# Optimization experiments

Measured on AMD Instinct MI355X. Metric: run time of the kernel, lower is better.

Reference implementation:

```python
import jax, jax.numpy as jnp
import numpy as np

B, N, D, H = 8, 1024, 512, 8  # batch, num_nodes, dim, num_heads
HD = D // H                    # head_dim = 64
N_VALID = 896                  # last 128 nodes per graph are padding


def setup_inputs() -> dict:
    key = jax.random.key(0)
    ks = jax.random.split(key, 6)
    x = jax.random.normal(ks[0], (B, N, D), dtype=jnp.float32)
    # boolean validity mask: some padding nodes so mask-fill / nan_to_num paths are hit
    mask = np.ones((B, N), dtype=bool)
    mask[:, N_VALID:] = False
    node_valid_mask = jnp.asarray(mask)
    attn_bias = jax.random.normal(ks[1], (B, H, N, N), dtype=jnp.float32) * 0.1
    # torch nn.Linear convention: y = x @ W.T + b
    qkv_w = jax.random.normal(ks[2], (3 * D, D), dtype=jnp.float32) * (D ** -0.5)
    qkv_b = jax.random.normal(ks[3], (3 * D,), dtype=jnp.float32) * 0.02
    out_w = jax.random.normal(ks[4], (D, D), dtype=jnp.float32) * (D ** -0.5)
    out_b = jax.random.normal(ks[5], (D,), dtype=jnp.float32) * 0.02
    return {"x": x, "node_valid_mask": node_valid_mask, "attn_bias": attn_bias,
            "qkv_w": qkv_w, "qkv_b": qkv_b, "out_w": out_w, "out_b": out_b}


def reference(x, node_valid_mask, attn_bias, qkv_w, qkv_b, out_w, out_b):
    b, n, d = x.shape
    scale = HD ** -0.5
    # qkv projection -> [3, B, H, N, HD]
    qkv = (x @ qkv_w.T + qkv_b).reshape(b, n, 3, H, HD).transpose(2, 0, 3, 1, 4)
    q, k, v = qkv[0], qkv[1], qkv[2]
    scores = jnp.einsum('bhqd,bhkd->bhqk', q, k) * scale + attn_bias  # [B,H,N,N]
    # pair mask: both query and key node must be valid
    pair_mask = node_valid_mask[:, :, None] & node_valid_mask[:, None, :]  # [B,N,N]
    scores = jnp.where(pair_mask[:, None, :, :], scores, -jnp.inf)
    attn = jax.nn.softmax(scores, axis=-1)
    # fully-masked query rows produce NaN -> zero, matching torch.nan_to_num
    attn = jnp.nan_to_num(attn, nan=0.0, posinf=0.0, neginf=0.0)
    out = jnp.einsum('bhqk,bhkd->bhqd', attn, v)        # [B,H,N,HD]
    out = out.transpose(0, 2, 1, 3).reshape(b, n, d)     # [B,N,D]
    return out @ out_w.T + out_b
```

## Files before the change

kernel.cpp:

```cpp
#include <hip/hip_runtime.h>
#include <math.h>

constexpr int Bc  = 8;
constexpr int Nn  = 1024;
constexpr int Dd  = 512;
constexpr int Hh  = 8;
constexpr int HD  = 64;
constexpr float SCALE = 0.125f;

typedef unsigned short ushort_t;
typedef unsigned int uint32;
typedef __attribute__((ext_vector_type(8))) short short8;
typedef __attribute__((ext_vector_type(4))) float f32x4;

__device__ __forceinline__ uint32 bf16rn(float x) {
  uint32 u = __float_as_uint(x);
  return (u + 0x7FFFu + ((u >> 16) & 1u)) >> 16;
}
__device__ __forceinline__ float bf16up(uint32 h) { return __uint_as_float(h << 16); }

__device__ __forceinline__ void split8(const float* xs, uint4& hi, uint4& lo) {
  uint32 h[8], l[8];
#pragma unroll
  for (int j = 0; j < 8; ++j) {
    h[j] = bf16rn(xs[j]);
    l[j] = bf16rn(xs[j] - bf16up(h[j]));
  }
  hi.x = h[0] | (h[1] << 16); hi.y = h[2] | (h[3] << 16);
  hi.z = h[4] | (h[5] << 16); hi.w = h[6] | (h[7] << 16);
  lo.x = l[0] | (l[1] << 16); lo.y = l[2] | (l[3] << 16);
  lo.z = l[4] | (l[5] << 16); lo.w = l[6] | (l[7] << 16);
}

__device__ __forceinline__ bool lane_valid(const unsigned char* m8, bool bytelay, int idx) {
  if (bytelay) return m8[idx] != 0;
  return ((const int*)m8)[idx] != 0;
}

__global__ __launch_bounds__(256) void convert_split(
    const float* __restrict__ src, ushort_t* __restrict__ dst)
{
  const int t    = blockIdx.x * 256 + threadIdx.x;
  const int lane = t & 63;
  const int blk  = t >> 6;
  const int rt   = blk >> 4, ks = blk & 15;
  const int row  = rt * 16 + (lane & 15);
  const int k    = ks * 32 + (lane >> 4) * 8;

  const float* s = src + (size_t)row * 512 + k;
  float4 a = *(const float4*)s, b = *(const float4*)(s + 4);
  float xs[8] = {a.x, a.y, a.z, a.w, b.x, b.y, b.z, b.w};
  uint4 hi, lo; split8(xs, hi, lo);

  ushort_t* d = dst + (size_t)blk * 1024 + lane * 8;
  *(uint4*)d = hi;
  *(uint4*)(d + 512) = lo;
}

__global__ __launch_bounds__(256) void convert_frag_qk(
    const float* __restrict__ src, ushort_t* __restrict__ dst)
{
  const int t    = blockIdx.x * 256 + threadIdx.x;
  const int lane = t & 63;
  const int fid  = t >> 6;
  const int tile = fid >> 1, ks = fid & 1;
  const int row  = tile * 16 + (lane & 15);
  const int d    = ks * 32 + (lane >> 4) * 8;

  const float* s = src + (size_t)row * HD + d;
  float4 a = *(const float4*)s, b = *(const float4*)(s + 4);
  float xs[8] = {a.x, a.y, a.z, a.w, b.x, b.y, b.z, b.w};
  uint4 hi, lo; split8(xs, hi, lo);

  ushort_t* dp = dst + (size_t)fid * 1024 + lane * 8;
  *(uint4*)dp = hi;
  *(uint4*)(dp + 512) = lo;
}

__global__ __launch_bounds__(256) void convert_frag_v(
    const float* __restrict__ src, ushort_t* __restrict__ dst)
{
  const int t    = blockIdx.x * 256 + threadIdx.x;
  const int lane = t & 63;
  const int fid  = t >> 6;
  const int dt   = fid & 3;
  const int ks   = (fid >> 2) & 1;
  const int kt   = (fid >> 3) & 15;
  const int bh   = fid >> 7;
  const int d    = dt * 16 + (lane & 15);
  const int key0 = kt * 64 + ks * 32 + (lane >> 4) * 8;

  const float* s = src + ((size_t)bh * Nn + key0) * HD + d;
  float xs[8];
#pragma unroll
  for (int j = 0; j < 8; ++j) xs[j] = s[(size_t)j * HD];
  uint4 hi, lo; split8(xs, hi, lo);

  ushort_t* dp = dst + (size_t)fid * 1024 + lane * 8;
  *(uint4*)dp = hi;
  *(uint4*)(dp + 512) = lo;
}

template<bool SCATTER>
__global__ __launch_bounds__(256) void gemm_x3(
    const ushort_t* __restrict__ Ac, const float* __restrict__ W,
    const float* __restrict__ bias, float* __restrict__ C, int Ncols,
    float* __restrict__ qb, float* __restrict__ kb, float* __restrict__ vb)
{
  __shared__ ushort_t Ablk[8 * 1024];
  __shared__ ushort_t Bblk[8 * 1024];

  const int t    = threadIdx.x;
  const int lane = t & 63, w = t >> 6;
  const int wr   = w >> 1, wc = w & 1;
  const int j0   = blockIdx.x * 128, i0 = blockIdx.y * 128;
  const int srow = t >> 2, skc = t & 3;

  f32x4 acc[4][4];
#pragma unroll
  for (int a = 0; a < 4; ++a)
#pragma unroll
    for (int b = 0; b < 4; ++b) acc[a][b] = (f32x4){0.f, 0.f, 0.f, 0.f};

  for (int kt = 0; kt < 16; ++kt) {
    __syncthreads();
#pragma unroll
    for (int i = 0; i < 4; ++i) {
      const int c = w * 4 + i, rt = c >> 1, hl = c & 1;
      const size_t goff =
          ((size_t)((i0 >> 4) + rt) * 16 + kt) * 1024 + hl * 512 + lane * 8;
      *(uint4*)&Ablk[rt * 1024 + hl * 512 + lane * 8] = *(const uint4*)&Ac[goff];
    }
#pragma unroll
    for (int p = 0; p < 2; ++p) {
      const int row = p * 64 + srow;
      const float* s = W + (size_t)(j0 + row) * 512 + kt * 32 + skc * 8;
      float4 w0 = *(const float4*)s, w1 = *(const float4*)(s + 4);
      float xs[8] = {w0.x, w0.y, w0.z, w0.w, w1.x, w1.y, w1.z, w1.w};
      uint4 hi, lo; split8(xs, hi, lo);
      ushort_t* d = &Bblk[(row >> 4) * 1024 + ((row & 15) + 16 * skc) * 8];
      *(uint4*)d = hi;
      *(uint4*)(d + 512) = lo;
    }
    __syncthreads();

    const ushort_t* Ab = &Ablk[(wr * 4) * 1024 + lane * 8];
    const ushort_t* Bb = &Bblk[(wc * 4) * 1024 + lane * 8];
    short8 Ah[4], Al[4];
#pragma unroll
    for (int ti = 0; ti < 4; ++ti) {
      Ah[ti] = *(const short8*)(Ab + ti * 1024);
      Al[ti] = *(const short8*)(Ab + ti * 1024 + 512);
    }
#pragma unroll
    for (int ct = 0; ct < 4; ++ct) {
      short8 Bh = *(const short8*)(Bb + ct * 1024);
      short8 Bl = *(const short8*)(Bb + ct * 1024 + 512);
#pragma unroll
      for (int ti = 0; ti < 4; ++ti) {
        acc[ti][ct] = __builtin_amdgcn_mfma_f32_16x16x32_bf16(Ah[ti], Bh, acc[ti][ct], 0, 0, 0);
        acc[ti][ct] = __builtin_amdgcn_mfma_f32_16x16x32_bf16(Al[ti], Bh, acc[ti][ct], 0, 0, 0);
        acc[ti][ct] = __builtin_amdgcn_mfma_f32_16x16x32_bf16(Ah[ti], Bl, acc[ti][ct], 0, 0, 0);
      }
    }
  }

  const int rbase = i0 + wr * 64 + (lane >> 4) * 4;
  const int cbase = j0 + wc * 64 + (lane & 15);
#pragma unroll
  for (int ct = 0; ct < 4; ++ct) {
    const int col = cbase + ct * 16;
    const float bv = bias[col];
    float* dst = nullptr;
    if (SCATTER) {
      const int s = col >> 9, h = (col >> 6) & 7;
      dst  = (s == 0) ? qb : (s == 1) ? kb : vb;
      dst += (size_t)h * Nn * HD + (col & 63);
    }
#pragma unroll
    for (int ti = 0; ti < 4; ++ti) {
      const int r0 = rbase + ti * 16;
#pragma unroll
      for (int r = 0; r < 4; ++r) {
        const float v = acc[ti][ct][r] + bv;
        const int row = r0 + r;
        if (SCATTER) {
          const int b2 = row >> 10, n = row & 1023;
          dst[((size_t)b2 * Hh * Nn + n) * HD] = v;
        } else {
          C[(size_t)row * Ncols + col] = v;
        }
      }
    }
  }
}

__global__ __launch_bounds__(256) void attn_mfma(
    const ushort_t* __restrict__ qf, const ushort_t* __restrict__ kf,
    const ushort_t* __restrict__ vf, const float* __restrict__ bias,
    const unsigned char* __restrict__ m8, float* __restrict__ outp)
{
  __shared__ ushort_t Pbuf[4][2048];

  const int t    = threadIdx.x;
  const int lane = t & 63, w = t >> 6;
  const int bx   = blockIdx.x;
  const int qt   = bx & 15;
  const int bh   = bx >> 4;
  const int b    = bh >> 3, h = bh & 7;
  const int tt   = qt * 4 + w;
  const int q0   = tt * 16;
  const bool bytelay = (m8[1] != 0);

  short8 Qh[2], Ql[2];
#pragma unroll
  for (int ks = 0; ks < 2; ++ks) {
    const ushort_t* qp = qf + ((size_t)(bh * 64 + tt) * 2 + ks) * 1024 + lane * 8;
    Qh[ks] = *(const short8*)qp;
    Ql[ks] = *(const short8*)(qp + 512);
  }

  f32x4 Oacc[4];
#pragma unroll
  for (int dt = 0; dt < 4; ++dt) Oacc[dt] = (f32x4){0.f, 0.f, 0.f, 0.f};
  float m_run[4], l_run[4];
#pragma unroll
  for (int r = 0; r < 4; ++r) { m_run[r] = -__builtin_inff(); l_run[r] = 0.f; }

  ushort_t* pb = &Pbuf[w][0];

  for (int kt = 0; kt < 16; ++kt) {
    const bool kvme = lane_valid(m8, bytelay, b * Nn + kt * 64 + lane);
    const unsigned long long kmask = __ballot(kvme);
    if (kmask == 0ull) continue;

    const float* bp = bias + ((size_t)bh * Nn + q0 + (lane >> 4) * 4) * Nn
                           + kt * 64 + (lane & 15);
    float bias_v[4][4];
#pragma unroll
    for (int r = 0; r < 4; ++r)
#pragma unroll
      for (int nt = 0; nt < 4; ++nt)
        bias_v[nt][r] = bp[(size_t)r * Nn + nt * 16];

    f32x4 Sacc[4];
#pragma unroll
    for (int nt = 0; nt < 4; ++nt) Sacc[nt] = (f32x4){0.f, 0.f, 0.f, 0.f};
#pragma unroll
    for (int ks = 0; ks < 2; ++ks)
#pragma unroll
      for (int nt = 0; nt < 4; ++nt) {
        const ushort_t* kp =
            kf + ((size_t)(bh * 64 + kt * 4 + nt) * 2 + ks) * 1024 + lane * 8;
        short8 Kh = *(const short8*)kp;
        short8 Kl = *(const short8*)(kp + 512);
        Sacc[nt] = __builtin_amdgcn_mfma_f32_16x16x32_bf16(Qh[ks], Kh, Sacc[nt], 0, 0, 0);
        Sacc[nt] = __builtin_amdgcn_mfma_f32_16x16x32_bf16(Ql[ks], Kh, Sacc[nt], 0, 0, 0);
        Sacc[nt] = __builtin_amdgcn_mfma_f32_16x16x32_bf16(Qh[ks], Kl, Sacc[nt], 0, 0, 0);
      }

    float Sv[4][4];
    float mt[4] = {-__builtin_inff(), -__builtin_inff(), -__builtin_inff(), -__builtin_inff()};
#pragma unroll
    for (int nt = 0; nt < 4; ++nt) {
      const bool kv = (kmask >> (nt * 16 + (lane & 15))) & 1ull;
#pragma unroll
      for (int r = 0; r < 4; ++r) {
        float s = kv ? Sacc[nt][r] * SCALE + bias_v[nt][r] : -__builtin_inff();
        Sv[nt][r] = s;
        mt[r] = fmaxf(mt[r], s);
      }
    }
#pragma unroll
    for (int off = 1; off < 16; off <<= 1)
#pragma unroll
      for (int r = 0; r < 4; ++r) mt[r] = fmaxf(mt[r], __shfl_xor(mt[r], off));

    float alpha[4], lt[4];
#pragma unroll
    for (int r = 0; r < 4; ++r) {
      const float mn = fmaxf(m_run[r], mt[r]);
      alpha[r] = __expf(m_run[r] - mn);
      m_run[r] = mn;
      lt[r] = 0.f;
    }
#pragma unroll
    for (int nt = 0; nt < 4; ++nt) {
      const int ksp    = nt >> 1;
      const int key_in = (nt & 1) * 16 + (lane & 15);
      const int lane_p = 16 * (key_in >> 3);
      const int j      = key_in & 7;
#pragma unroll
      for (int r = 0; r < 4; ++r) {
        const float p = __expf(Sv[nt][r] - m_run[r]);
        lt[r] += p;
        const uint32 ph = bf16rn(p);
        const uint32 pl = bf16rn(p - bf16up(ph));
        const int lp = ((lane >> 4) * 4 + r) + lane_p;
        pb[(ksp * 2 + 0) * 512 + lp * 8 + j] = (ushort_t)ph;
        pb[(ksp * 2 + 1) * 512 + lp * 8 + j] = (ushort_t)pl;
      }
    }
#pragma unroll
    for (int off = 1; off < 16; off <<= 1)
#pragma unroll
      for (int r = 0; r < 4; ++r) lt[r] += __shfl_xor(lt[r], off);
#pragma unroll
    for (int r = 0; r < 4; ++r) l_run[r] = l_run[r] * alpha[r] + lt[r];
#pragma unroll
    for (int dt = 0; dt < 4; ++dt)
#pragma unroll
      for (int r = 0; r < 4; ++r) Oacc[dt][r] *= alpha[r];

    short8 Ph[2], Pl[2];
#pragma unroll
    for (int ks = 0; ks < 2; ++ks) {
      Ph[ks] = *(const short8*)&pb[(ks * 2 + 0) * 512 + lane * 8];
      Pl[ks] = *(const short8*)&pb[(ks * 2 + 1) * 512 + lane * 8];
    }

#pragma unroll
    for (int dt = 0; dt < 4; ++dt)
#pragma unroll
      for (int ks = 0; ks < 2; ++ks) {
        const ushort_t* vp =
            vf + ((size_t)(((bh * 16 + kt) * 2 + ks) * 4 + dt)) * 1024 + lane * 8;
        short8 Vh = *(const short8*)vp;
        short8 Vl = *(const short8*)(vp + 512);
        Oacc[dt] = __builtin_amdgcn_mfma_f32_16x16x32_bf16(Ph[ks], Vh, Oacc[dt], 0, 0, 0);
        Oacc[dt] = __builtin_amdgcn_mfma_f32_16x16x32_bf16(Pl[ks], Vh, Oacc[dt], 0, 0, 0);
        Oacc[dt] = __builtin_amdgcn_mfma_f32_16x16x32_bf16(Ph[ks], Vl, Oacc[dt], 0, 0, 0);
      }
  }

#pragma unroll
  for (int r = 0; r < 4; ++r) {
    const int q = q0 + (lane >> 4) * 4 + r;
    const bool vq = lane_valid(m8, bytelay, b * Nn + q);
    const float rinv = (vq && l_run[r] > 0.f) ? (1.f / l_run[r]) : 0.f;
    float* op = outp + ((size_t)(b * Nn + q)) * Dd + h * HD + (lane & 15);
#pragma unroll
    for (int dt = 0; dt < 4; ++dt) op[dt * 16] = Oacc[dt][r] * rinv;
  }
}

extern "C" void kernel_launch(void* const* d_in, const int* in_sizes, int n_in,
                              void* d_out, int out_size, void* d_ws, size_t ws_size,
                              hipStream_t stream) {
  const float* x        = (const float*)d_in[0];
  const unsigned char* mask8 = (const unsigned char*)d_in[1];
  const float* attnbias = (const float*)d_in[2];
  const float* qkv_w    = (const float*)d_in[3];
  const float* qkv_b    = (const float*)d_in[4];
  const float* out_w    = (const float*)d_in[5];
  const float* out_b    = (const float*)d_in[6];
  float* out = (float*)d_out;

  float* ws = (float*)d_ws;
  const size_t SEG = (size_t)Bc * Hh * Nn * HD;
  float* A = ws;
  float* B = ws + SEG;
  float* C = ws + 2 * SEG;
  float* D = ws + 3 * SEG;

  ushort_t* x_conv    = (ushort_t*)A;
  float*    qbuf      = B;
  float*    kbuf      = C;
  float*    vbuf      = D;
  ushort_t* qfrag     = (ushort_t*)A;
  ushort_t* kfrag     = (ushort_t*)B;
  ushort_t* vfrag     = (ushort_t*)C;
  float*    aout      = D;
  ushort_t* aout_conv = (ushort_t*)A;

  convert_split<<<2048, 256, 0, stream>>>(x, x_conv);

  gemm_x3<true><<<dim3(12, 64), 256, 0, stream>>>(
      x_conv, qkv_w, qkv_b, nullptr, 1536, qbuf, kbuf, vbuf);

  convert_frag_qk<<<2048, 256, 0, stream>>>(qbuf, qfrag);
  convert_frag_qk<<<2048, 256, 0, stream>>>(kbuf, kfrag);
  convert_frag_v <<<2048, 256, 0, stream>>>(vbuf, vfrag);

  attn_mfma<<<1024, 256, 0, stream>>>(
      qfrag, kfrag, vfrag, attnbias, mask8, aout);

  convert_split<<<2048, 256, 0, stream>>>(aout, aout_conv);
  gemm_x3<false><<<dim3(4, 64), 256, 0, stream>>>(
      aout_conv, out_w, out_b, out, 512, nullptr, nullptr, nullptr);
}
```

Before: 566.9 us.

## Pre-split weights into bf16 fragments, prefetch attention bias, narrow output GEMM tile

Weights are now converted once per call into hi/lo bf16 fragment layout by convert_split, so the GEMM inner loop only copies pre-split fragments instead of re-splitting fp32 weights in every block. The attention kernel prefetches the next key tile's bias with coalesced float4 loads into registers and stages it through shared memory, replacing strided scalar bias loads. The output GEMM uses a 64-wide column tile, which gives 512 blocks instead of 256. The cost is extra conversion launches and scratch use of d_out and workspace for the weight fragments.

Result: slower. 741.3 us (+30.8%).

```diff
diff --git a/kernel.cpp b/kernel.cpp
--- a/kernel.cpp
+++ b/kernel.cpp
@@ -101,51 +101,48 @@
   *(uint4*)(dp + 512) = lo;
 }
 
-template<bool SCATTER>
-__global__ __launch_bounds__(256) void gemm_x3(
-    const ushort_t* __restrict__ Ac, const float* __restrict__ W,
+template<int BN, bool SCATTER>
+__global__ __launch_bounds__(256) void gemm_f(
+    const ushort_t* __restrict__ Ac, const ushort_t* __restrict__ Bfrag,
     const float* __restrict__ bias, float* __restrict__ C, int Ncols,
     float* __restrict__ qb, float* __restrict__ kb, float* __restrict__ vb)
 {
-  __shared__ ushort_t Ablk[8 * 1024];
-  __shared__ ushort_t Bblk[8 * 1024];
-
-  const int t    = threadIdx.x;
-  const int lane = t & 63, w = t >> 6;
-  const int wr   = w >> 1, wc = w & 1;
-  const int j0   = blockIdx.x * 128, i0 = blockIdx.y * 128;
-  const int srow = t >> 2, skc = t & 3;
-
-  f32x4 acc[4][4];
+  constexpr int NT   = BN / 32;
+  constexpr int BCH  = (BN / 16) * 2;
+  __shared__ ushort_t Ablk[16 * 512];
+  __shared__ ushort_t Bblk[BCH * 512];
+
+  const int t = threadIdx.x, lane = t & 63, w = t >> 6;
+  const int wr = w >> 1, wc = w & 1;
+  const int j0 = blockIdx.x * BN, i0 = blockIdx.y * 128;
+
+  f32x4 acc[4][NT];
 #pragma unroll
   for (int a = 0; a < 4; ++a)
 #pragma unroll
-    for (int b = 0; b < 4; ++b) acc[a][b] = (f32x4){0.f, 0.f, 0.f, 0.f};
+    for (int b = 0; b < NT; ++b) acc[a][b] = (f32x4){0.f, 0.f, 0.f, 0.f};
 
   for (int kt = 0; kt < 16; ++kt) {
     __syncthreads();
 #pragma unroll
-    for (int i = 0; i < 4; ++i) {
-      const int c = w * 4 + i, rt = c >> 1, hl = c & 1;
-      const size_t goff =
-          ((size_t)((i0 >> 4) + rt) * 16 + kt) * 1024 + hl * 512 + lane * 8;
-      *(uint4*)&Ablk[rt * 1024 + hl * 512 + lane * 8] = *(const uint4*)&Ac[goff];
-    }
-#pragma unroll
-    for (int p = 0; p < 2; ++p) {
-      const int row = p * 64 + srow;
-      const float* s = W + (size_t)(j0 + row) * 512 + kt * 32 + skc * 8;
-      float4 w0 = *(const float4*)s, w1 = *(const float4*)(s + 4);
-      float xs[8] = {w0.x, w0.y, w0.z, w0.w, w1.x, w1.y, w1.z, w1.w};
-      uint4 hi, lo; split8(xs, hi, lo);
-      ushort_t* d = &Bblk[(row >> 4) * 1024 + ((row & 15) + 16 * skc) * 8];
-      *(uint4*)d = hi;
-      *(uint4*)(d + 512) = lo;
+    for (int ci = 0; ci < (16 + BCH) / 4; ++ci) {
+      const int c = ci * 4 + w;
+      const ushort_t* src;
+      ushort_t* dst;
+      if (c < 16) {
+        const int rt = c >> 1, hl = c & 1;
+        src = Ac + (((size_t)((i0 >> 4) + rt) * 16 + kt)) * 1024 + hl * 512 + lane * 8;
+        dst = Ablk + c * 512 + lane * 8;
+      } else {
+        const int cb = c - 16, bt = cb >> 1, hl = cb & 1;
+        src = Bfrag + (((size_t)((j0 >> 4) + bt) * 16 + kt)) * 1024 + hl * 512 + lane * 8;
+        dst = Bblk + cb * 512 + lane * 8;
+      }
+      *(uint4*)dst = *(const uint4*)src;
     }
     __syncthreads();
 
-    const ushort_t* Ab = &Ablk[(wr * 4) * 1024 + lane * 8];
-    const ushort_t* Bb = &Bblk[(wc * 4) * 1024 + lane * 8];
+    const ushort_t* Ab = Ablk + (size_t)(wr * 4) * 1024 + lane * 8;
     short8 Ah[4], Al[4];
 #pragma unroll
     for (int ti = 0; ti < 4; ++ti) {
@@ -153,9 +150,10 @@
       Al[ti] = *(const short8*)(Ab + ti * 1024 + 512);
     }
 #pragma unroll
-    for (int ct = 0; ct < 4; ++ct) {
-      short8 Bh = *(const short8*)(Bb + ct * 1024);
-      short8 Bl = *(const short8*)(Bb + ct * 1024 + 512);
+    for (int ct = 0; ct < NT; ++ct) {
+      const ushort_t* Bb = Bblk + (size_t)(wc * NT + ct) * 1024 + lane * 8;
+      short8 Bh = *(const short8*)Bb;
+      short8 Bl = *(const short8*)(Bb + 512);
 #pragma unroll
       for (int ti = 0; ti < 4; ++ti) {
         acc[ti][ct] = __builtin_amdgcn_mfma_f32_16x16x32_bf16(Ah[ti], Bh, acc[ti][ct], 0, 0, 0);
@@ -166,10 +164,10 @@
   }
 
   const int rbase = i0 + wr * 64 + (lane >> 4) * 4;
-  const int cbase = j0 + wc * 64 + (lane & 15);
-#pragma unroll
-  for (int ct = 0; ct < 4; ++ct) {
-    const int col = cbase + ct * 16;
+  const int cb0   = j0 + wc * (NT * 16) + (lane & 15);
+#pragma unroll
+  for (int ct = 0; ct < NT; ++ct) {
+    const int col = cb0 + ct * 16;
     const float bv = bias[col];
     float* dst = nullptr;
     if (SCATTER) {
@@ -200,16 +198,14 @@
     const ushort_t* __restrict__ vf, const float* __restrict__ bias,
     const unsigned char* __restrict__ m8, float* __restrict__ outp)
 {
-  __shared__ ushort_t Pbuf[4][2048];
-
-  const int t    = threadIdx.x;
-  const int lane = t & 63, w = t >> 6;
-  const int bx   = blockIdx.x;
-  const int qt   = bx & 15;
-  const int bh   = bx >> 4;
-  const int b    = bh >> 3, h = bh & 7;
-  const int tt   = qt * 4 + w;
-  const int q0   = tt * 16;
+  __shared__ float sbuf[4][2][1088];
+
+  const int t = threadIdx.x, lane = t & 63, w = t >> 6;
+  const int bx = blockIdx.x;
+  const int qt = bx & 15, bh = bx >> 4;
+  const int b = bh >> 3, h = bh & 7;
+  const int tt = qt * 4 + w;
+  const int q0 = tt * 16;
   const bool bytelay = (m8[1] != 0);
 
   short8 Qh[2], Ql[2];
@@ -227,110 +223,134 @@
 #pragma unroll
   for (int r = 0; r < 4; ++r) { m_run[r] = -__builtin_inff(); l_run[r] = 0.f; }
 
-  ushort_t* pb = &Pbuf[w][0];
+  float*    bb = &sbuf[w][0][0];
+  ushort_t* pb = (ushort_t*)&sbuf[w][1][0];
+
+  const float* bp0 = bias + ((size_t)bh * Nn + q0 + (lane >> 4) * 4) * Nn + (lane & 15) * 4;
+
+  unsigned long long km_cur = __ballot(lane_valid(m8, bytelay, b * Nn + lane));
+  float4 breg[4] = {};
+  if (km_cur) {
+#pragma unroll
+    for (int i = 0; i < 4; ++i) breg[i] = *(const float4*)(bp0 + (size_t)i * Nn);
+  }
 
   for (int kt = 0; kt < 16; ++kt) {
-    const bool kvme = lane_valid(m8, bytelay, b * Nn + kt * 64 + lane);
-    const unsigned long long kmask = __ballot(kvme);
-    if (kmask == 0ull) continue;
-
-    const float* bp = bias + ((size_t)bh * Nn + q0 + (lane >> 4) * 4) * Nn
-                           + kt * 64 + (lane & 15);
-    float bias_v[4][4];
-#pragma unroll
-    for (int r = 0; r < 4; ++r)
+    unsigned long long km_next = 0ull;
+    if (kt < 15)
+      km_next = __ballot(lane_valid(m8, bytelay, b * Nn + (kt + 1) * 64 + lane));
+    float4 bnext[4] = {};
+    if (km_next) {
+      const float* bp = bp0 + (size_t)(kt + 1) * 64;
+#pragma unroll
+      for (int i = 0; i < 4; ++i) bnext[i] = *(const float4*)(bp + (size_t)i * Nn);
+    }
+
+    if (km_cur) {
+#pragma unroll
+      for (int i = 0; i < 4; ++i)
+        *(float4*)&bb[((lane >> 4) * 4 + i) * 68 + (lane & 15) * 4] = breg[i];
+
+      f32x4 Sacc[4];
+#pragma unroll
+      for (int nt = 0; nt < 4; ++nt) Sacc[nt] = (f32x4){0.f, 0.f, 0.f, 0.f};
+#pragma unroll
+      for (int ks = 0; ks < 2; ++ks)
+#pragma unroll
+        for (int nt = 0; nt < 4; ++nt) {
+          const ushort_t* kp =
+              kf + ((size_t)(bh * 64 + kt * 4 + nt) * 2 + ks) * 1024 + lane * 8;
+          short8 Kh = *(const short8*)kp;
+          short8 Kl = *(const short8*)(kp + 512);
+          Sacc[nt] = __builtin_amdgcn_mfma_f32_16x16x32_bf16(Qh[ks], Kh, Sacc[nt], 0, 0, 0);
+          Sacc[nt] = __builtin_amdgcn_mfma_f32_16x16x32_bf16(Ql[ks], Kh, Sacc[nt], 0, 0, 0);
+          Sacc[nt] = __builtin_amdgcn_mfma_f32_16x16x32_bf16(Qh[ks], Kl, Sacc[nt], 0, 0, 0);
+        }
+
+      float bias_v[4][4];
 #pragma unroll
       for (int nt = 0; nt < 4; ++nt)
-        bias_v[nt][r] = bp[(size_t)r * Nn + nt * 16];
-
-    f32x4 Sacc[4];
-#pragma unroll
-    for (int nt = 0; nt < 4; ++nt) Sacc[nt] = (f32x4){0.f, 0.f, 0.f, 0.f};
-#pragma unroll
-    for (int ks = 0; ks < 2; ++ks)
+#pragma unroll
+        for (int r = 0; r < 4; ++r)
+          bias_v[nt][r] = bb[((lane >> 4) * 4 + r) * 68 + nt * 16 + (lane & 15)];
+
+      float Sv[4][4];
+      float mt[4] = {-__builtin_inff(), -__builtin_inff(), -__builtin_inff(), -__builtin_inff()};
 #pragma unroll
       for (int nt = 0; nt < 4; ++nt) {
-        const ushort_t* kp =
-            kf + ((size_t)(bh * 64 + kt * 4 + nt) * 2 + ks) * 1024 + lane * 8;
-        short8 Kh = *(const short8*)kp;
-        short8 Kl = *(const short8*)(kp + 512);
-        Sacc[nt] = __builtin_amdgcn_mfma_f32_16x16x32_bf16(Qh[ks], Kh, Sacc[nt], 0, 0, 0);
-        Sacc[nt] = __builtin_amdgcn_mfma_f32_16x16x32_bf16(Ql[ks], Kh, Sacc[nt], 0, 0, 0);
-        Sacc[nt] = __builtin_amdgcn_mfma_f32_16x16x32_bf16(Qh[ks], Kl, Sacc[nt], 0, 0, 0);
-      }
-
-    float Sv[4][4];
-    float mt[4] = {-__builtin_inff(), -__builtin_inff(), -__builtin_inff(), -__builtin_inff()};
-#pragma unroll
-    for (int nt = 0; nt < 4; ++nt) {
-      const bool kv = (kmask >> (nt * 16 + (lane & 15))) & 1ull;
+        const bool kv = (km_cur >> (nt * 16 + (lane & 15))) & 1ull;
+#pragma unroll
+        for (int r = 0; r < 4; ++r) {
+          float s = kv ? Sacc[nt][r] * SCALE + bias_v[nt][r] : -__builtin_inff();
+          Sv[nt][r] = s;
+          mt[r] = fmaxf(mt[r], s);
+        }
+      }
+#pragma unroll
+      for (int off = 1; off < 16; off <<= 1)
+#pragma unroll
+        for (int r = 0; r < 4; ++r) mt[r] = fmaxf(mt[r], __shfl_xor(mt[r], off));
+
+      float alpha[4], lt[4];
 #pragma unroll
       for (int r = 0; r < 4; ++r) {
-        float s = kv ? Sacc[nt][r] * SCALE + bias_v[nt][r] : -__builtin_inff();
-        Sv[nt][r] = s;
-        mt[r] = fmaxf(mt[r], s);
-      }
-    }
-#pragma unroll
-    for (int off = 1; off < 16; off <<= 1)
-#pragma unroll
-      for (int r = 0; r < 4; ++r) mt[r] = fmaxf(mt[r], __shfl_xor(mt[r], off));
-
-    float alpha[4], lt[4];
-#pragma unroll
-    for (int r = 0; r < 4; ++r) {
-      const float mn = fmaxf(m_run[r], mt[r]);
-      alpha[r] = __expf(m_run[r] - mn);
-      m_run[r] = mn;
-      lt[r] = 0.f;
-    }
-#pragma unroll
-    for (int nt = 0; nt < 4; ++nt) {
-      const int ksp    = nt >> 1;
-      const int key_in = (nt & 1) * 16 + (lane & 15);
-      const int lane_p = 16 * (key_in >> 3);
-      const int j      = key_in & 7;
-#pragma unroll
-      for (int r = 0; r < 4; ++r) {
-        const float p = __expf(Sv[nt][r] - m_run[r]);
-        lt[r] += p;
-        const uint32 ph = bf16rn(p);
-        const uint32 pl = bf16rn(p - bf16up(ph));
-        const int lp = ((lane >> 4) * 4 + r) + lane_p;
-        pb[(ksp * 2 + 0) * 512 + lp * 8 + j] = (ushort_t)ph;
-        pb[(ksp * 2 + 1) * 512 + lp * 8 + j] = (ushort_t)pl;
-      }
-    }
-#pragma unroll
-    for (int off = 1; off < 16; off <<= 1)
-#pragma unroll
-      for (int r = 0; r < 4; ++r) lt[r] += __shfl_xor(lt[r], off);
-#pragma unroll
-    for (int r = 0; r < 4; ++r) l_run[r] = l_run[r] * alpha[r] + lt[r];
-#pragma unroll
-    for (int dt = 0; dt < 4; ++dt)
-#pragma unroll
-      for (int r = 0; r < 4; ++r) Oacc[dt][r] *= alpha[r];
-
-    short8 Ph[2], Pl[2];
-#pragma unroll
-    for (int ks = 0; ks < 2; ++ks) {
-      Ph[ks] = *(const short8*)&pb[(ks * 2 + 0) * 512 + lane * 8];
-      Pl[ks] = *(const short8*)&pb[(ks * 2 + 1) * 512 + lane * 8];
-    }
-
-#pragma unroll
-    for (int dt = 0; dt < 4; ++dt)
+        const float mn = fmaxf(m_run[r], mt[r]);
+        alpha[r] = __expf(m_run[r] - mn);
+        m_run[r] = mn;
+        lt[r] = 0.f;
+      }
+#pragma unroll
+      for (int nt = 0; nt < 4; ++nt) {
+        const int ksp    = nt >> 1;
+        const int key_in = (nt & 1) * 16 + (lane & 15);
+        const int lane_p = 16 * (key_in >> 3);
+        const int j      = key_in & 7;
+#pragma unroll
+        for (int r = 0; r < 4; ++r) {
+          const float p = __expf(Sv[nt][r] - m_run[r]);
+          lt[r] += p;
+          const uint32 ph = bf16rn(p);
+          const uint32 pl = bf16rn(p - bf16up(ph));
+          const int lp = ((lane >> 4) * 4 + r) + lane_p;
+          pb[(ksp * 2 + 0) * 512 + lp * 8 + j] = (ushort_t)ph;
+          pb[(ksp * 2 + 1) * 512 + lp * 8 + j] = (ushort_t)pl;
+        }
+      }
+#pragma unroll
+      for (int off = 1; off < 16; off <<= 1)
+#pragma unroll
+        for (int r = 0; r < 4; ++r) lt[r] += __shfl_xor(lt[r], off);
+#pragma unroll
+      for (int r = 0; r < 4; ++r) l_run[r] = l_run[r] * alpha[r] + lt[r];
+#pragma unroll
+      for (int dt = 0; dt < 4; ++dt)
+#pragma unroll
+        for (int r = 0; r < 4; ++r) Oacc[dt][r] *= alpha[r];
+
+      short8 Ph[2], Pl[2];
 #pragma unroll
       for (int ks = 0; ks < 2; ++ks) {
-        const ushort_t* vp =
-            vf + ((size_t)(((bh * 16 + kt) * 2 + ks) * 4 + dt)) * 1024 + lane * 8;
-        short8 Vh = *(const short8*)vp;
-        short8 Vl = *(const short8*)(vp + 512);
-        Oacc[dt] = __builtin_amdgcn_mfma_f32_16x16x32_bf16(Ph[ks], Vh, Oacc[dt], 0, 0, 0);
-        Oacc[dt] = __builtin_amdgcn_mfma_f32_16x16x32_bf16(Pl[ks], Vh, Oacc[dt], 0, 0, 0);
-        Oacc[dt] = __builtin_amdgcn_mfma_f32_16x16x32_bf16(Ph[ks], Vl, Oacc[dt], 0, 0, 0);
-      }
+        Ph[ks] = *(const short8*)&pb[(ks * 2 + 0) * 512 + lane * 8];
+        Pl[ks] = *(const short8*)&pb[(ks * 2 + 1) * 512 + lane * 8];
+      }
+
+#pragma unroll
+      for (int dt = 0; dt < 4; ++dt)
+#pragma unroll
+        for (int ks = 0; ks < 2; ++ks) {
+          const ushort_t* vp =
+              vf + ((size_t)(((bh * 16 + kt) * 2 + ks) * 4 + dt)) * 1024 + lane * 8;
+          short8 Vh = *(const short8*)vp;
+          short8 Vl = *(const short8*)(vp + 512);
+          Oacc[dt] = __builtin_amdgcn_mfma_f32_16x16x32_bf16(Ph[ks], Vh, Oacc[dt], 0, 0, 0);
+          Oacc[dt] = __builtin_amdgcn_mfma_f32_16x16x32_bf16(Pl[ks], Vh, Oacc[dt], 0, 0, 0);
+          Oacc[dt] = __builtin_amdgcn_mfma_f32_16x16x32_bf16(Ph[ks], Vl, Oacc[dt], 0, 0, 0);
+        }
+    }
+
+    km_cur = km_next;
+#pragma unroll
+    for (int i = 0; i < 4; ++i) breg[i] = bnext[i];
   }
 
 #pragma unroll
@@ -372,11 +392,14 @@
   ushort_t* vfrag     = (ushort_t*)C;
   float*    aout      = D;
   ushort_t* aout_conv = (ushort_t*)A;
+  ushort_t* qkv_wf    = (ushort_t*)d_out;
+  ushort_t* out_wf    = (ushort_t*)B;
 
   convert_split<<<2048, 256, 0, stream>>>(x, x_conv);
-
-  gemm_x3<true><<<dim3(12, 64), 256, 0, stream>>>(
-      x_conv, qkv_w, qkv_b, nullptr, 1536, qbuf, kbuf, vbuf);
+  convert_split<<<384, 256, 0, stream>>>(qkv_w, qkv_wf);
+
+  gemm_f<128, true><<<dim3(12, 64), 256, 0, stream>>>(
+      x_conv, qkv_wf, qkv_b, nullptr, 1536, qbuf, kbuf, vbuf);
 
   convert_frag_qk<<<2048, 256, 0, stream>>>(qbuf, qfrag);
   convert_frag_qk<<<2048, 256, 0, stream>>>(kbuf, kfrag);
@@ -385,7 +408,8 @@
   attn_mfma<<<1024, 256, 0, stream>>>(
       qfrag, kfrag, vfrag, attnbias, mask8, aout);
 
+  convert_split<<<128, 256, 0, stream>>>(out_w, out_wf);
   convert_split<<<2048, 256, 0, stream>>>(aout, aout_conv);
-  gemm_x3<false><<<dim3(4, 64), 256, 0, stream>>>(
-      aout_conv, out_w, out_b, out, 512, nullptr, nullptr, nullptr);
-}
+  gemm_f<64, false><<<dim3(8, 64), 256, 0, stream>>>(
+      aout_conv, out_wf, out_b, out, 512, nullptr, nullptr, nullptr);
+}
```
